# Performance work log

Hardware: AMD Instinct MI355X
Metric: run time of the kernel (lower is better)

Reference implementation:

```python
import jax, jax.numpy as jnp
import numpy as np

B, H, N = 128, 512, 1024

def setup_inputs() -> dict:
    key = jax.random.key(0)
    ks = jax.random.split(key, 9)
    s = 1.0 / np.sqrt(H)
    return {
        "mc_hidden": jax.random.normal(ks[0], (B, H), jnp.float32),
        "sn_hidden": jax.random.normal(ks[1], (B, H, N), jnp.float32),
        "attn_W": jax.random.normal(ks[2], (H, 2 * H), jnp.float32) * s,
        "attn_v": jax.random.normal(ks[3], (H,), jnp.float32) * s,
        "ptr_v": jax.random.normal(ks[4], (H,), jnp.float32) * s,
        "fc1_W": jax.random.normal(ks[5], (H, 2 * H), jnp.float32) * s,
        "fc1_b": jax.random.normal(ks[6], (H,), jnp.float32) * s,
        "fc2_W": jax.random.normal(ks[7], (H, H), jnp.float32) * s,
        "fc2_b": jax.random.normal(ks[8], (H,), jnp.float32) * s,
    }


def reference(mc_hidden, sn_hidden, attn_W, attn_v, ptr_v, fc1_W, fc1_b, fc2_W, fc2_b):
    # ---- Attention (Bahdanau-style additive scoring) ----
    # hidden: (B, 2H, N) = cat(sn_hidden, mc expanded along N) on dim 1
    mc_exp = jnp.broadcast_to(mc_hidden[:, :, None], sn_hidden.shape)  # (B,H,N)
    hidden = jnp.concatenate((sn_hidden, mc_exp), axis=1)              # (B,2H,N)
    # W @ hidden -> (B,H,N); v @ tanh(.) -> (B,N)
    scores = jnp.einsum('h,bhn->bn', attn_v,
                        jnp.tanh(jnp.einsum('hk,bkn->bhn', attn_W, hidden)))
    attns = jax.nn.softmax(scores, axis=-1)                            # (B,N)
    # ---- Context + pointer scoring ----
    context = jnp.einsum('bn,bhn->bh', attns, sn_hidden)               # (B,H)
    x = jnp.concatenate((mc_hidden, context), axis=1)                  # (B,2H)
    out = jax.nn.relu(x @ fc1_W.T + fc1_b)                             # (B,H)
    out = jax.nn.relu(out @ fc2_W.T + fc2_b)                           # (B,H)
    probs = jnp.einsum('h,bhn->bn', ptr_v,
                       jnp.tanh(sn_hidden + out[:, :, None]))          # (B,N)
    return probs
```

## Files before the change

kernel.cpp:

```cpp
#include <hip/hip_runtime.h>
#include <hip/hip_bf16.h>

#define Bn 128
#define Hd 512
#define Nn 1024

typedef __attribute__((ext_vector_type(8))) short short8;
typedef __attribute__((ext_vector_type(4))) float f32x4;

#define GLOAD_LDS16(gptr, lptr)                                                     \
    __builtin_amdgcn_global_load_lds(                                               \
        (const __attribute__((address_space(1))) void*)(gptr),                      \
        (__attribute__((address_space(3))) void*)(lptr), 16, 0, 0)

__device__ __forceinline__ float bf2f(unsigned u) {
    unsigned v = u << 16;
    float f;
    __builtin_memcpy(&f, &v, 4);
    return f;
}

__device__ __forceinline__ unsigned short f2bf(float f) {
    unsigned x;
    __builtin_memcpy(&x, &f, 4);
    unsigned r = x + 0x7fffu + ((x >> 16) & 1u);
    return (unsigned short)(r >> 16);
}

__device__ __forceinline__ float wave_sum(float v) {
    v += __shfl_xor(v, 32);
    v += __shfl_xor(v, 16);
    v += __shfl_xor(v, 8);
    v += __shfl_xor(v, 4);
    v += __shfl_xor(v, 2);
    v += __shfl_xor(v, 1);
    return v;
}

__device__ __forceinline__ float tanh_fast(float x) {
    float e = __expf(2.0f * x);
    return 1.0f - 2.0f * __builtin_amdgcn_rcpf(e + 1.0f);
}

__global__ void convert_W_kernel(const float* __restrict__ attn_W,
                                 unsigned short* __restrict__ Wb) {
    int idx = (blockIdx.x * 256 + threadIdx.x) * 8;
    int h = idx >> 9;
    int k = idx & 511;
    const float* p = attn_W + (size_t)h * 1024 + k;
    float4 v0 = *(const float4*)p;
    float4 v1 = *(const float4*)(p + 4);
    unsigned short t[8] = {f2bf(v0.x), f2bf(v0.y), f2bf(v0.z), f2bf(v0.w),
                           f2bf(v1.x), f2bf(v1.y), f2bf(v1.z), f2bf(v1.w)};
    *(uint4*)(Wb + idx) = *(uint4*)t;
}

__global__ void transpose_sn_kernel(const float* __restrict__ sn,
                                    unsigned short* __restrict__ snT) {
    __shared__ unsigned ldsb[32 * 132];
    int bid = blockIdx.x;
    int b = bid >> 6;
    int kt = (bid >> 3) & 7;
    int nt = bid & 7;
    int k0 = kt << 6, n0 = nt << 7;
    int t = threadIdx.x;

    int kp_l = t >> 5;
    int n4 = (t & 31) * 4;
#pragma unroll
    for (int j = 0; j < 4; ++j) {
        int kp = j * 8 + kp_l;
        const float* p0 = sn + ((size_t)(b * Hd + k0 + 2 * kp)) * Nn + n0 + n4;
        float4 f0 = *(const float4*)p0;
        float4 f1 = *(const float4*)(p0 + Nn);
        unsigned u[4];
        u[0] = (unsigned)f2bf(f0.x) | ((unsigned)f2bf(f1.x) << 16);
        u[1] = (unsigned)f2bf(f0.y) | ((unsigned)f2bf(f1.y) << 16);
        u[2] = (unsigned)f2bf(f0.z) | ((unsigned)f2bf(f1.z) << 16);
        u[3] = (unsigned)f2bf(f0.w) | ((unsigned)f2bf(f1.w) << 16);
        *(uint4*)&ldsb[kp * 132 + n4] = *(uint4*)u;
    }
    __syncthreads();

    int c = t & 7;
#pragma unroll
    for (int it = 0; it < 4; ++it) {
        int n = (t >> 3) + it * 32;
        unsigned u[4];
#pragma unroll
        for (int i = 0; i < 4; ++i) u[i] = ldsb[(c * 4 + i) * 132 + n];
        unsigned short* dst = snT + ((size_t)(b * Nn) + n0 + n) * Hd + k0 + c * 8;
        *(uint4*)dst = *(uint4*)u;
    }
}

__global__ void mc_term_kernel(const float* __restrict__ mc,
                               const float* __restrict__ attn_W,
                               float* __restrict__ mc_term) {
    int wg = (blockIdx.x * blockDim.x + threadIdx.x) >> 6;
    int lane = threadIdx.x & 63;
    int b = wg >> 9;
    int h = wg & 511;
    const float* m = mc + b * Hd + lane * 8;
    const float* w = attn_W + (size_t)h * 1024 + 512 + lane * 8;
    float4 m0 = *(const float4*)m, m1 = *(const float4*)(m + 4);
    float4 w0 = *(const float4*)w, w1 = *(const float4*)(w + 4);
    float acc = m0.x * w0.x + m0.y * w0.y + m0.z * w0.z + m0.w * w0.w +
                m1.x * w1.x + m1.y * w1.y + m1.z * w1.z + m1.w * w1.w;
    acc = wave_sum(acc);
    if (lane == 0) mc_term[b * Hd + h] = acc;
}

__global__ __launch_bounds__(256, 2)
void attn_score_kernel(const unsigned short* __restrict__ snT,
                       const unsigned short* __restrict__ Wb,
                       const float* __restrict__ attn_v,
                       const float* __restrict__ mc_term,
                       float* __restrict__ scores) {
    __shared__ __align__(16) unsigned short A_lds[512 * 64];
    __shared__ __align__(16) unsigned short B_lds[64 * 64];
    __shared__ float av_s[512];
    __shared__ float mct_s[512];
    __shared__ float ssum[64];

    const int b = blockIdx.x >> 4;
    const int n0 = (blockIdx.x & 15) << 6;
    const int tid = threadIdx.x;
    const int lane = tid & 63;
    const int wid = tid >> 6;
    const int quad = lane >> 4;
    const int l15 = lane & 15;
    const int m0 = wid * 128;

    av_s[tid] = attn_v[tid];
    av_s[tid + 256] = attn_v[tid + 256];
    mct_s[tid] = mc_term[b * Hd + tid];
    mct_s[tid + 256] = mc_term[b * Hd + tid + 256];
    if (tid < 64) ssum[tid] = 0.f;

    f32x4 acc[8][4];
#pragma unroll
    for (int i = 0; i < 8; ++i)
#pragma unroll
        for (int j = 0; j < 4; ++j) {
            f32x4 z = {0.f, 0.f, 0.f, 0.f};
            acc[i][j] = z;
        }

    const int r8 = lane >> 3;
    const int csw = ((lane & 7) ^ r8) * 16;
    const char* Wg = (const char*)Wb;
    const char* Bg = (const char*)snT + ((size_t)(b * Nn + n0)) * 1024;
    const int key = l15 & 7;

    for (int k0 = 0; k0 < 512; k0 += 64) {
#pragma unroll
        for (int i = 0; i < 16; ++i) {
            const int row = m0 + i * 8;
            GLOAD_LDS16(Wg + (size_t)(row + r8) * 1024 + k0 * 2 + csw,
                        (char*)A_lds + row * 128);
        }
#pragma unroll
        for (int i = 0; i < 2; ++i) {
            const int row = wid * 16 + i * 8;
            GLOAD_LDS16(Bg + (size_t)(row + r8) * 1024 + k0 * 2 + csw,
                        (char*)B_lds + row * 128);
        }
        __syncthreads();
#pragma unroll
        for (int kk = 0; kk < 2; ++kk) {
            const int cb = quad + kk * 4;
            short8 bfr[4], afr[8];
#pragma unroll
            for (int nt = 0; nt < 4; ++nt) {
                const int n = nt * 16 + l15;
                bfr[nt] = *(const short8*)((const char*)B_lds + n * 128 + ((cb ^ key) * 16));
            }
#pragma unroll
            for (int mt = 0; mt < 8; ++mt) {
                const int m = m0 + mt * 16 + l15;
                afr[mt] = *(const short8*)((const char*)A_lds + m * 128 + ((cb ^ key) * 16));
            }
#pragma unroll
            for (int mt = 0; mt < 8; ++mt)
#pragma unroll
                for (int nt = 0; nt < 4; ++nt)
                    acc[mt][nt] = __builtin_amdgcn_mfma_f32_16x16x32_bf16(afr[mt], bfr[nt], acc[mt][nt], 0, 0, 0);
        }
        __syncthreads();
    }

    float s[4] = {0.f, 0.f, 0.f, 0.f};
#pragma unroll
    for (int mt = 0; mt < 8; ++mt) {
        int hb = m0 + mt * 16 + quad * 4;
#pragma unroll
        for (int r = 0; r < 4; ++r) {
            float av = av_s[hb + r];
            float mcv = mct_s[hb + r];
#pragma unroll
            for (int nt = 0; nt < 4; ++nt)
                s[nt] += av * tanh_fast(acc[mt][nt][r] + mcv);
        }
    }
#pragma unroll
    for (int nt = 0; nt < 4; ++nt) {
        float v = s[nt];
        v += __shfl_xor(v, 16);
        v += __shfl_xor(v, 32);
        if (lane < 16) atomicAdd(&ssum[nt * 16 + l15], v);
    }
    __syncthreads();
    if (tid < 64) scores[b * Nn + n0 + tid] = ssum[tid];
}

__global__ void softmax_kernel(float* __restrict__ scores) {
    const int b = blockIdx.x;
    const int tid = threadIdx.x;
    const int lane = tid & 63, wid = tid >> 6;
    __shared__ float red[4];
    float v[4];
#pragma unroll
    for (int i = 0; i < 4; ++i) v[i] = scores[b * Nn + tid + i * 256];
    float m = fmaxf(fmaxf(v[0], v[1]), fmaxf(v[2], v[3]));
#pragma unroll
    for (int off = 32; off >= 1; off >>= 1) m = fmaxf(m, __shfl_xor(m, off));
    if (lane == 0) red[wid] = m;
    __syncthreads();
    m = fmaxf(fmaxf(red[0], red[1]), fmaxf(red[2], red[3]));
    __syncthreads();
    float s = 0.f;
#pragma unroll
    for (int i = 0; i < 4; ++i) {
        v[i] = __expf(v[i] - m);
        s += v[i];
    }
    s = wave_sum(s);
    if (lane == 0) red[wid] = s;
    __syncthreads();
    s = red[0] + red[1] + red[2] + red[3];
    float inv = __builtin_amdgcn_rcpf(s);
#pragma unroll
    for (int i = 0; i < 4; ++i) scores[b * Nn + tid + i * 256] = v[i] * inv;
}

__global__ void context_kernel(const unsigned short* __restrict__ snT,
                               const float* __restrict__ attns,
                               float* __restrict__ context) {
    int b = blockIdx.x >> 3;
    int nc = (blockIdx.x & 7) << 7;
    int t = threadIdx.x;
    __shared__ float a_s[128];
    if (t < 128) a_s[t] = attns[b * Nn + nc + t];
    __syncthreads();
    const unsigned short* base = snT + ((size_t)(b * Nn) + nc) * Hd + t * 2;
    float acc0 = 0.f, acc1 = 0.f;
#pragma unroll 4
    for (int i = 0; i < 128; ++i) {
        unsigned d = *(const unsigned*)(base + (size_t)i * Hd);
        float a = a_s[i];
        acc0 += a * bf2f(d & 0xffffu);
        acc1 += a * bf2f(d >> 16);
    }
    atomicAdd(&context[b * Hd + 2 * t], acc0);
    atomicAdd(&context[b * Hd + 2 * t + 1], acc1);
}

__global__ void fc1_kernel(const float* __restrict__ mc,
                           const float* __restrict__ ctx,
                           const float* __restrict__ fc1_W,
                           const float* __restrict__ fc1_b,
                           float* __restrict__ out1) {
    int wg = (blockIdx.x * blockDim.x + threadIdx.x) >> 6;
    int lane = threadIdx.x & 63;
    int b = wg >> 9, h = wg & 511;
    const float* wr = fc1_W + (size_t)h * 1024;
    float acc = 0.f;
    {
        float4 w0 = *(const float4*)(wr + lane * 8);
        float4 w1 = *(const float4*)(wr + lane * 8 + 4);
        float4 x0 = *(const float4*)(mc + b * Hd + lane * 8);
        float4 x1 = *(const float4*)(mc + b * Hd + lane * 8 + 4);
        acc += w0.x * x0.x + w0.y * x0.y + w0.z * x0.z + w0.w * x0.w;
        acc += w1.x * x1.x + w1.y * x1.y + w1.z * x1.z + w1.w * x1.w;
    }
    {
        float4 w0 = *(const float4*)(wr + 512 + lane * 8);
        float4 w1 = *(const float4*)(wr + 512 + lane * 8 + 4);
        float4 x0 = *(const float4*)(ctx + b * Hd + lane * 8);
        float4 x1 = *(const float4*)(ctx + b * Hd + lane * 8 + 4);
        acc += w0.x * x0.x + w0.y * x0.y + w0.z * x0.z + w0.w * x0.w;
        acc += w1.x * x1.x + w1.y * x1.y + w1.z * x1.z + w1.w * x1.w;
    }
    acc = wave_sum(acc);
    if (lane == 0) out1[b * Hd + h] = fmaxf(acc + fc1_b[h], 0.f);
}

__global__ void fc2_kernel(const float* __restrict__ out1,
                           const float* __restrict__ fc2_W,
                           const float* __restrict__ fc2_b,
                           float* __restrict__ out2) {
    int wg = (blockIdx.x * blockDim.x + threadIdx.x) >> 6;
    int lane = threadIdx.x & 63;
    int b = wg >> 9, h = wg & 511;
    const float* wr = fc2_W + (size_t)h * 512 + lane * 8;
    float4 w0 = *(const float4*)wr;
    float4 w1 = *(const float4*)(wr + 4);
    float4 x0 = *(const float4*)(out1 + b * Hd + lane * 8);
    float4 x1 = *(const float4*)(out1 + b * Hd + lane * 8 + 4);
    float acc = w0.x * x0.x + w0.y * x0.y + w0.z * x0.z + w0.w * x0.w +
                w1.x * x1.x + w1.y * x1.y + w1.z * x1.z + w1.w * x1.w;
    acc = wave_sum(acc);
    if (lane == 0) out2[b * Hd + h] = fmaxf(acc + fc2_b[h], 0.f);
}

__global__ void final_kernel(const unsigned short* __restrict__ snT,
                             const float* __restrict__ ptr_v,
                             const float* __restrict__ out2,
                             float* __restrict__ probs) {
    int b = blockIdx.x >> 4;
    int n0 = (blockIdx.x & 15) << 6;
    int t = threadIdx.x;
    int n = n0 + (t >> 2), p = t & 3;
    __shared__ float pv_s[512], o2_s[512];
    pv_s[t] = ptr_v[t];
    pv_s[t + 256] = ptr_v[t + 256];
    o2_s[t] = out2[b * Hd + t];
    o2_s[t + 256] = out2[b * Hd + t + 256];
    __syncthreads();
    const unsigned short* row = snT + ((size_t)(b * Nn) + n) * Hd + p * 8;
    float a = 0.f;
#pragma unroll 4
    for (int j = 0; j < 16; ++j) {
        uint4 d = *(const uint4*)(row + j * 32);
        int hb = p * 8 + j * 32;
        const unsigned* u = (const unsigned*)&d;
#pragma unroll
        for (int q = 0; q < 4; ++q) {
            int h = hb + q * 2;
            float x0 = bf2f(u[q] & 0xffffu);
            float x1 = bf2f(u[q] >> 16);
            a += pv_s[h] * tanh_fast(x0 + o2_s[h]);
            a += pv_s[h + 1] * tanh_fast(x1 + o2_s[h + 1]);
        }
    }
    a += __shfl_xor(a, 1);
    a += __shfl_xor(a, 2);
    if (p == 0) probs[b * Nn + n] = a;
}

extern "C" void kernel_launch(void* const* d_in, const int* in_sizes, int n_in,
                              void* d_out, int out_size, void* d_ws, size_t ws_size,
                              hipStream_t stream) {
    const float* mc  = (const float*)d_in[0];
    const float* sn  = (const float*)d_in[1];
    const float* aW  = (const float*)d_in[2];
    const float* av  = (const float*)d_in[3];
    const float* pv  = (const float*)d_in[4];
    const float* f1W = (const float*)d_in[5];
    const float* f1b = (const float*)d_in[6];
    const float* f2W = (const float*)d_in[7];
    const float* f2b = (const float*)d_in[8];

    unsigned short* snT = (unsigned short*)d_ws;
    unsigned short* Wb  = snT + (size_t)Bn * Nn * Hd;
    float* fws     = (float*)(Wb + 512 * 512);
    float* mc_term = fws;
    float* scores  = mc_term + Bn * Hd;
    float* context = scores + Bn * Nn;
    float* out1    = context + Bn * Hd;
    float* out2    = out1 + Bn * Hd;
    float* probs   = (float*)d_out;

    hipMemsetAsync(context, 0, Bn * Hd * sizeof(float), stream);
    convert_W_kernel<<<dim3(128), dim3(256), 0, stream>>>(aW, Wb);
    transpose_sn_kernel<<<dim3(8192), dim3(256), 0, stream>>>(sn, snT);
    mc_term_kernel<<<dim3(16384), dim3(256), 0, stream>>>(mc, aW, mc_term);
    attn_score_kernel<<<dim3(2048), dim3(256), 0, stream>>>(snT, Wb, av, mc_term, scores);
    softmax_kernel<<<dim3(128), dim3(256), 0, stream>>>(scores);
    context_kernel<<<dim3(1024), dim3(256), 0, stream>>>(snT, scores, context);
    fc1_kernel<<<dim3(16384), dim3(256), 0, stream>>>(mc, context, f1W, f1b, out1);
    fc2_kernel<<<dim3(16384), dim3(256), 0, stream>>>(out1, f2W, f2b, out2);
    final_kernel<<<dim3(2048), dim3(256), 0, stream>>>(snT, pv, out2, probs);
}
```

Baseline: 565.7 us.

## Retile attention GEMM to 256x128, fuse softmax into context, use packed bf16 conversion

The attention score kernel now splits H into two halves per block and widens the N tile to 128. LDS shrinks from about 72KB to 48KB, and the W tile is reloaded fewer times per batch row. Partial scores from the two H halves are combined with global atomics into a zero-initialised buffer. The softmax kernel is folded into the context kernel: each block recomputes the row max and sum redundantly, which removes one launch. The fp32-to-bf16 conversion also switches to the packed intrinsic.

```diff
diff --git a/kernel.cpp b/kernel.cpp
--- a/kernel.cpp
+++ b/kernel.cpp
@@ -25,6 +25,13 @@
     __builtin_memcpy(&x, &f, 4);
     unsigned r = x + 0x7fffu + ((x >> 16) & 1u);
     return (unsigned short)(r >> 16);
+}
+
+__device__ __forceinline__ unsigned pack_bf2(float a, float b) {
+    __hip_bfloat162 h = __float22bfloat162_rn(float2{a, b});
+    unsigned u;
+    __builtin_memcpy(&u, &h, 4);
+    return u;
 }
 
 __device__ __forceinline__ float wave_sum(float v) {
@@ -50,9 +57,9 @@
     const float* p = attn_W + (size_t)h * 1024 + k;
     float4 v0 = *(const float4*)p;
     float4 v1 = *(const float4*)(p + 4);
-    unsigned short t[8] = {f2bf(v0.x), f2bf(v0.y), f2bf(v0.z), f2bf(v0.w),
-                           f2bf(v1.x), f2bf(v1.y), f2bf(v1.z), f2bf(v1.w)};
-    *(uint4*)(Wb + idx) = *(uint4*)t;
+    unsigned u[4] = {pack_bf2(v0.x, v0.y), pack_bf2(v0.z, v0.w),
+                     pack_bf2(v1.x, v1.y), pack_bf2(v1.z, v1.w)};
+    *(uint4*)(Wb + idx) = *(uint4*)u;
 }
 
 __global__ void transpose_sn_kernel(const float* __restrict__ sn,
@@ -74,10 +81,10 @@
         float4 f0 = *(const float4*)p0;
         float4 f1 = *(const float4*)(p0 + Nn);
         unsigned u[4];
-        u[0] = (unsigned)f2bf(f0.x) | ((unsigned)f2bf(f1.x) << 16);
-        u[1] = (unsigned)f2bf(f0.y) | ((unsigned)f2bf(f1.y) << 16);
-        u[2] = (unsigned)f2bf(f0.z) | ((unsigned)f2bf(f1.z) << 16);
-        u[3] = (unsigned)f2bf(f0.w) | ((unsigned)f2bf(f1.w) << 16);
+        u[0] = pack_bf2(f0.x, f1.x);
+        u[1] = pack_bf2(f0.y, f1.y);
+        u[2] = pack_bf2(f0.z, f1.z);
+        u[3] = pack_bf2(f0.w, f1.w);
         *(uint4*)&ldsb[kp * 132 + n4] = *(uint4*)u;
     }
     __syncthreads();
@@ -117,52 +124,51 @@
                        const float* __restrict__ attn_v,
                        const float* __restrict__ mc_term,
                        float* __restrict__ scores) {
-    __shared__ __align__(16) unsigned short A_lds[512 * 64];
-    __shared__ __align__(16) unsigned short B_lds[64 * 64];
-    __shared__ float av_s[512];
-    __shared__ float mct_s[512];
-    __shared__ float ssum[64];
-
-    const int b = blockIdx.x >> 4;
-    const int n0 = (blockIdx.x & 15) << 6;
+    __shared__ __align__(16) unsigned short A_lds[256 * 64];
+    __shared__ __align__(16) unsigned short B_lds[128 * 64];
+    __shared__ float av_s[256];
+    __shared__ float mct_s[256];
+    __shared__ float ssum[128];
+
+    const int bid = blockIdx.x;
+    const int b = bid >> 4;
+    const int mh = (bid >> 3) & 1;
+    const int n0 = (bid & 7) << 7;
     const int tid = threadIdx.x;
     const int lane = tid & 63;
     const int wid = tid >> 6;
     const int quad = lane >> 4;
     const int l15 = lane & 15;
-    const int m0 = wid * 128;
-
-    av_s[tid] = attn_v[tid];
-    av_s[tid + 256] = attn_v[tid + 256];
-    mct_s[tid] = mc_term[b * Hd + tid];
-    mct_s[tid + 256] = mc_term[b * Hd + tid + 256];
-    if (tid < 64) ssum[tid] = 0.f;
-
-    f32x4 acc[8][4];
-#pragma unroll
-    for (int i = 0; i < 8; ++i)
-#pragma unroll
-        for (int j = 0; j < 4; ++j) {
+
+    av_s[tid] = attn_v[mh * 256 + tid];
+    mct_s[tid] = mc_term[b * Hd + mh * 256 + tid];
+    if (tid < 128) ssum[tid] = 0.f;
+
+    f32x4 acc[4][8];
+#pragma unroll
+    for (int i = 0; i < 4; ++i)
+#pragma unroll
+        for (int j = 0; j < 8; ++j) {
             f32x4 z = {0.f, 0.f, 0.f, 0.f};
             acc[i][j] = z;
         }
 
     const int r8 = lane >> 3;
     const int csw = ((lane & 7) ^ r8) * 16;
-    const char* Wg = (const char*)Wb;
+    const char* Wg = (const char*)Wb + (size_t)(mh * 256) * 1024;
     const char* Bg = (const char*)snT + ((size_t)(b * Nn + n0)) * 1024;
     const int key = l15 & 7;
 
     for (int k0 = 0; k0 < 512; k0 += 64) {
 #pragma unroll
-        for (int i = 0; i < 16; ++i) {
-            const int row = m0 + i * 8;
+        for (int i = 0; i < 8; ++i) {
+            const int row = wid * 64 + i * 8;
             GLOAD_LDS16(Wg + (size_t)(row + r8) * 1024 + k0 * 2 + csw,
                         (char*)A_lds + row * 128);
         }
 #pragma unroll
-        for (int i = 0; i < 2; ++i) {
-            const int row = wid * 16 + i * 8;
+        for (int i = 0; i < 4; ++i) {
+            const int row = wid * 32 + i * 8;
             GLOAD_LDS16(Bg + (size_t)(row + r8) * 1024 + k0 * 2 + csw,
                         (char*)B_lds + row * 128);
         }
@@ -170,89 +176,81 @@
 #pragma unroll
         for (int kk = 0; kk < 2; ++kk) {
             const int cb = quad + kk * 4;
-            short8 bfr[4], afr[8];
-#pragma unroll
-            for (int nt = 0; nt < 4; ++nt) {
+            short8 bfr[8], afr[4];
+#pragma unroll
+            for (int nt = 0; nt < 8; ++nt) {
                 const int n = nt * 16 + l15;
                 bfr[nt] = *(const short8*)((const char*)B_lds + n * 128 + ((cb ^ key) * 16));
             }
 #pragma unroll
-            for (int mt = 0; mt < 8; ++mt) {
-                const int m = m0 + mt * 16 + l15;
+            for (int mt = 0; mt < 4; ++mt) {
+                const int m = wid * 64 + mt * 16 + l15;
                 afr[mt] = *(const short8*)((const char*)A_lds + m * 128 + ((cb ^ key) * 16));
             }
 #pragma unroll
-            for (int mt = 0; mt < 8; ++mt)
-#pragma unroll
-                for (int nt = 0; nt < 4; ++nt)
+            for (int mt = 0; mt < 4; ++mt)
+#pragma unroll
+                for (int nt = 0; nt < 8; ++nt)
                     acc[mt][nt] = __builtin_amdgcn_mfma_f32_16x16x32_bf16(afr[mt], bfr[nt], acc[mt][nt], 0, 0, 0);
         }
         __syncthreads();
     }
 
-    float s[4] = {0.f, 0.f, 0.f, 0.f};
-#pragma unroll
-    for (int mt = 0; mt < 8; ++mt) {
-        int hb = m0 + mt * 16 + quad * 4;
+    float s[8] = {0.f, 0.f, 0.f, 0.f, 0.f, 0.f, 0.f, 0.f};
+#pragma unroll
+    for (int mt = 0; mt < 4; ++mt) {
+        int hb = wid * 64 + mt * 16 + quad * 4;
 #pragma unroll
         for (int r = 0; r < 4; ++r) {
             float av = av_s[hb + r];
             float mcv = mct_s[hb + r];
 #pragma unroll
-            for (int nt = 0; nt < 4; ++nt)
+            for (int nt = 0; nt < 8; ++nt)
                 s[nt] += av * tanh_fast(acc[mt][nt][r] + mcv);
         }
     }
 #pragma unroll
-    for (int nt = 0; nt < 4; ++nt) {
+    for (int nt = 0; nt < 8; ++nt) {
         float v = s[nt];
         v += __shfl_xor(v, 16);
         v += __shfl_xor(v, 32);
         if (lane < 16) atomicAdd(&ssum[nt * 16 + l15], v);
     }
     __syncthreads();
-    if (tid < 64) scores[b * Nn + n0 + tid] = ssum[tid];
-}
-
-__global__ void softmax_kernel(float* __restrict__ scores) {
-    const int b = blockIdx.x;
-    const int tid = threadIdx.x;
-    const int lane = tid & 63, wid = tid >> 6;
-    __shared__ float red[4];
-    float v[4];
-#pragma unroll
-    for (int i = 0; i < 4; ++i) v[i] = scores[b * Nn + tid + i * 256];
-    float m = fmaxf(fmaxf(v[0], v[1]), fmaxf(v[2], v[3]));
-#pragma unroll
-    for (int off = 32; off >= 1; off >>= 1) m = fmaxf(m, __shfl_xor(m, off));
-    if (lane == 0) red[wid] = m;
-    __syncthreads();
-    m = fmaxf(fmaxf(red[0], red[1]), fmaxf(red[2], red[3]));
-    __syncthreads();
-    float s = 0.f;
-#pragma unroll
-    for (int i = 0; i < 4; ++i) {
-        v[i] = __expf(v[i] - m);
-        s += v[i];
-    }
-    s = wave_sum(s);
-    if (lane == 0) red[wid] = s;
-    __syncthreads();
-    s = red[0] + red[1] + red[2] + red[3];
-    float inv = __builtin_amdgcn_rcpf(s);
-#pragma unroll
-    for (int i = 0; i < 4; ++i) scores[b * Nn + tid + i * 256] = v[i] * inv;
-}
-
-__global__ void context_kernel(const unsigned short* __restrict__ snT,
-                               const float* __restrict__ attns,
-                               float* __restrict__ context) {
+    if (tid < 128) atomicAdd(&scores[b * Nn + n0 + tid], ssum[tid]);
+}
+
+__global__ void softmax_context_kernel(const unsigned short* __restrict__ snT,
+                                       const float* __restrict__ scores,
+                                       float* __restrict__ context) {
     int b = blockIdx.x >> 3;
     int nc = (blockIdx.x & 7) << 7;
     int t = threadIdx.x;
+    int lane = t & 63, wid = t >> 6;
+    __shared__ float red[4];
     __shared__ float a_s[128];
-    if (t < 128) a_s[t] = attns[b * Nn + nc + t];
-    __syncthreads();
+
+    float v[4];
+#pragma unroll
+    for (int i = 0; i < 4; ++i) v[i] = scores[b * Nn + t + i * 256];
+    float m = fmaxf(fmaxf(v[0], v[1]), fmaxf(v[2], v[3]));
+#pragma unroll
+    for (int off = 32; off >= 1; off >>= 1) m = fmaxf(m, __shfl_xor(m, off));
+    if (lane == 0) red[wid] = m;
+    __syncthreads();
+    m = fmaxf(fmaxf(red[0], red[1]), fmaxf(red[2], red[3]));
+    __syncthreads();
+    float s = 0.f;
+#pragma unroll
+    for (int i = 0; i < 4; ++i) s += __expf(v[i] - m);
+    s = wave_sum(s);
+    if (lane == 0) red[wid] = s;
+    __syncthreads();
+    s = red[0] + red[1] + red[2] + red[3];
+    float inv = __builtin_amdgcn_rcpf(s);
+    if (t < 128) a_s[t] = __expf(scores[b * Nn + nc + t] - m) * inv;
+    __syncthreads();
+
     const unsigned short* base = snT + ((size_t)(b * Nn) + nc) * Hd + t * 2;
     float acc0 = 0.f, acc1 = 0.f;
 #pragma unroll 4
@@ -372,13 +370,12 @@
     float* out2    = out1 + Bn * Hd;
     float* probs   = (float*)d_out;
 
-    hipMemsetAsync(context, 0, Bn * Hd * sizeof(float), stream);
+    hipMemsetAsync(scores, 0, (Bn * Nn + Bn * Hd) * sizeof(float), stream);
     convert_W_kernel<<<dim3(128), dim3(256), 0, stream>>>(aW, Wb);
     transpose_sn_kernel<<<dim3(8192), dim3(256), 0, stream>>>(sn, snT);
     mc_term_kernel<<<dim3(16384), dim3(256), 0, stream>>>(mc, aW, mc_term);
     attn_score_kernel<<<dim3(2048), dim3(256), 0, stream>>>(snT, Wb, av, mc_term, scores);
-    softmax_kernel<<<dim3(128), dim3(256), 0, stream>>>(scores);
-    context_kernel<<<dim3(1024), dim3(256), 0, stream>>>(snT, scores, context);
+    softmax_context_kernel<<<dim3(1024), dim3(256), 0, stream>>>(snT, scores, context);
     fc1_kernel<<<dim3(16384), dim3(256), 0, stream>>>(mc, context, f1W, f1b, out1);
     fc2_kernel<<<dim3(16384), dim3(256), 0, stream>>>(out1, f2W, f2b, out2);
     final_kernel<<<dim3(2048), dim3(256), 0, stream>>>(snT, pv, out2, probs);
```

Measured after the change: 552.7 us. 2.3% less time.
